# Kernel tuning notes

Hardware: AMD Instinct MI355X
Metric: run time of the kernel (lower is better)

Reference implementation:

```python
import jax, jax.numpy as jnp
import numpy as np

N_NODES = 50000
N_EDGES = 800000
N_GRAPHS = 2048
NODE_F = 30
EDGE_F = 8
HID = 32
HEADS = 4
NEG_SLOPE = 0.2


def _gat_conv(x, src, dst, eattr, W, a_src, a_dst, We, a_edge, b):
    # x: [N, Fin]; src/dst: [E'] (self-loops already appended); eattr: [E', edge_dim]
    N = x.shape[0]
    H, C = a_src.shape
    h = (x @ W).reshape(N, H, C)                     # [N,H,C]
    e = (eattr @ We).reshape(-1, H, C)               # [E',H,C]
    al_s = jnp.sum(h * a_src, axis=-1)               # [N,H]
    al_d = jnp.sum(h * a_dst, axis=-1)               # [N,H]
    al_e = jnp.sum(e * a_edge, axis=-1)              # [E',H]
    alpha = al_s[src] + al_d[dst] + al_e             # [E',H]
    alpha = jax.nn.leaky_relu(alpha, NEG_SLOPE)
    # segment softmax over destination nodes (every node has a self-loop)
    mx = jax.ops.segment_max(alpha, dst, num_segments=N)
    alpha = jnp.exp(alpha - mx[dst])
    den = jax.ops.segment_sum(alpha, dst, num_segments=N)
    alpha = alpha / (den[dst] + 1e-16)
    msg = h[src] * alpha[:, :, None]                 # [E',H,C]
    out = jax.ops.segment_sum(msg, dst, num_segments=N)  # [N,H,C]
    return out.reshape(N, H * C) + b


def _make_params(key):
    ks = jax.random.split(key, 32)
    i = 0
    p = {}
    def nxt(shape, scale=0.1):
        nonlocal i
        k = ks[i]; i += 1
        return jax.random.normal(k, shape, dtype=jnp.float32) * scale
    dims = [(NODE_F, HEADS * HID), (HEADS * HID, HEADS * HID), (HEADS * HID, HEADS * HID)]
    for li, (fin, fout) in enumerate(dims, 1):
        p[f"W{li}"] = nxt((fin, fout))
        p[f"att_src{li}"] = nxt((HEADS, HID))
        p[f"att_dst{li}"] = nxt((HEADS, HID))
        p[f"We{li}"] = nxt((EDGE_F, HEADS * HID))
        p[f"att_e{li}"] = nxt((HEADS, HID))
        p[f"b{li}"] = nxt((HEADS * HID,))
    p["lw1"] = nxt((HEADS * HID, HID)); p["lb1"] = nxt((HID,))
    p["lw2"] = nxt((HID, HID)); p["lb2"] = nxt((HID,))
    p["lw3"] = nxt((HID, 1)); p["lb3"] = nxt((1,))
    return p


def setup_inputs() -> dict:
    key = jax.random.key(0)
    k1, k2, k3, k4, k5 = jax.random.split(key, 5)
    x = jax.random.normal(k1, (N_NODES, NODE_F), dtype=jnp.float32)
    edge_index = jax.random.randint(k2, (2, N_EDGES), 0, N_NODES, dtype=jnp.int64)
    edge_features = jax.random.normal(k3, (N_EDGES, EDGE_F), dtype=jnp.float32)
    batch = jnp.sort(jax.random.randint(k4, (N_NODES,), 0, N_GRAPHS, dtype=jnp.int64))
    inp = {"x": x, "edge_index": edge_index, "edge_features": edge_features, "batch": batch}
    inp.update(_make_params(k5))
    return inp


def reference(x, edge_index, edge_features, batch,
              W1, att_src1, att_dst1, We1, att_e1, b1,
              W2, att_src2, att_dst2, We2, att_e2, b2,
              W3, att_src3, att_dst3, We3, att_e3, b3,
              lw1, lb1, lw2, lb2, lw3, lb3):
    N = x.shape[0]
    # add self-loops (PyG GATConv default); self-loop edge_attr = mean of edge_attr
    loop = jnp.arange(N, dtype=edge_index.dtype)
    src = jnp.concatenate([edge_index[0], loop])
    dst = jnp.concatenate([edge_index[1], loop])
    mean_e = jnp.mean(edge_features, axis=0, keepdims=True)
    eattr = jnp.concatenate([edge_features, jnp.broadcast_to(mean_e, (N, EDGE_F))], axis=0)

    h = jax.nn.relu(_gat_conv(x, src, dst, eattr, W1, att_src1, att_dst1, We1, att_e1, b1))
    h = jax.nn.relu(_gat_conv(h, src, dst, eattr, W2, att_src2, att_dst2, We2, att_e2, b2))
    h = jax.nn.relu(_gat_conv(h, src, dst, eattr, W3, att_src3, att_dst3, We3, att_e3, b3))
    # global_add_pool
    g = jax.ops.segment_sum(h, batch, num_segments=N_GRAPHS)   # [G, H*C]
    g = jax.nn.relu(g @ lw1 + lb1)
    g = jax.nn.relu(g @ lw2 + lb2)
    g = jax.nn.relu(g @ lw3 + lb3)                              # [G, 1]
    return g
```

## Files before the change

kernel.cpp:

```cpp
#include <hip/hip_runtime.h>

#define NND 50000
#define NE  800000
#define NET 850000
#define NG  2048
#define SCB 196
#define MB  1024

typedef __attribute__((ext_vector_type(8))) short short8;
typedef __attribute__((ext_vector_type(4))) float float4v;

__device__ __forceinline__ float frelu(float v){ return v > 0.f ? v : 0.f; }

__device__ __forceinline__ unsigned short f2bf(float f){
    unsigned int u = __float_as_uint(f);
    u += 0x7FFFu + ((u >> 16) & 1u);
    return (unsigned short)(u >> 16);
}

__global__ __launch_bounds__(256) void k_mean(const float4* __restrict__ ef4,
                                              float* __restrict__ partial){
    __shared__ float4 red[256];
    int t = threadIdx.x;
    int i0 = blockIdx.x * 256 + t;
    const int S = MB * 256;
    float4 a = make_float4(0.f, 0.f, 0.f, 0.f);
    for (int j = i0; j < NE * 2; j += S){
        float4 v = ef4[j];
        a.x += v.x; a.y += v.y; a.z += v.z; a.w += v.w;
    }
    red[t] = a;
    __syncthreads();
    for (int off = 128; off >= 2; off >>= 1){
        if (t < off){
            float4 o = red[t + off];
            float4 m = red[t];
            m.x += o.x; m.y += o.y; m.z += o.z; m.w += o.w;
            red[t] = m;
        }
        __syncthreads();
    }
    if (t < 8){
        float v = (t < 4) ? ((const float*)&red[0])[t]
                          : ((const float*)&red[1])[t - 4];
        partial[blockIdx.x * 8 + t] = v;
    }
}

__global__ void k_prep(const float* __restrict__ partial,
                       const float* __restrict__ We1, const float* __restrict__ ae1,
                       const float* __restrict__ We2, const float* __restrict__ ae2,
                       const float* __restrict__ We3, const float* __restrict__ ae3,
                       float* __restrict__ M, float* __restrict__ sc){
    __shared__ float me[8];
    __shared__ float pm[16][8];
    __shared__ float Ms[96];
    int t = threadIdx.x;
    {
        int ch = t & 7, seg = t >> 3;
        float s = 0.f;
        for (int j = seg; j < MB; j += 16) s += partial[j * 8 + ch];
        pm[seg][ch] = s;
    }
    __syncthreads();
    if (t < 8){
        float s = 0.f;
        for (int i = 0; i < 16; i++) s += pm[i][t];
        me[t] = s * (1.0f / NE);
    }
    if (t < 96){
        int l = t >> 5, f = (t >> 2) & 7, h = t & 3;
        const float* We = (l == 0) ? We1 : ((l == 1) ? We2 : We3);
        const float* ae = (l == 0) ? ae1 : ((l == 1) ? ae2 : ae3);
        float s = 0.f;
        for (int c = 0; c < 32; c++) s += We[f * 128 + h * 32 + c] * ae[h * 32 + c];
        M[t] = s; Ms[t] = s;
    }
    __syncthreads();
    if (t < 12){
        int l = t >> 2, h = t & 3;
        float s = 0.f;
        for (int f = 0; f < 8; f++) s += me[f] * Ms[l * 32 + f * 4 + h];
        sc[t] = s;
    }
}

template<int FIN, int FINR>
__global__ __launch_bounds__(256) void k_gemm(
        const float* __restrict__ x, const float* __restrict__ W,
        const float* __restrict__ asrc, const float* __restrict__ adst,
        unsigned short* __restrict__ h, float* __restrict__ als,
        float* __restrict__ ald){
    constexpr int KS = FIN + 8;
    constexpr int SZ1 = 64 * KS + 128 * KS;
    constexpr int SZ2 = 64 * 136;
    constexpr int LSZ = SZ1 > SZ2 ? SZ1 : SZ2;
    __shared__ unsigned short lds[LSZ];
    unsigned short* xa = lds;
    unsigned short* wb = lds + 64 * KS;
    int t = threadIdx.x;
    int r0 = blockIdx.x * 64;

    for (int i = t; i < 64 * (FIN / 2); i += 256){
        int r = i / (FIN / 2), kp = i % (FIN / 2);
        int gr = r0 + r, k = 2 * kp;
        float v0 = 0.f, v1 = 0.f;
        if (gr < NND){
            if (k     < FINR) v0 = x[gr * FINR + k];
            if (k + 1 < FINR) v1 = x[gr * FINR + k + 1];
        }
        unsigned int pk = (unsigned int)f2bf(v0) | ((unsigned int)f2bf(v1) << 16);
        *(unsigned int*)&xa[r * KS + k] = pk;
    }
    for (int i = t; i < 128 * (FIN / 2); i += 256){
        int n = i & 127, kp = i >> 7, k = 2 * kp;
        float v0 = (k     < FINR) ? W[k * 128 + n]       : 0.f;
        float v1 = (k + 1 < FINR) ? W[(k + 1) * 128 + n] : 0.f;
        unsigned int pk = (unsigned int)f2bf(v0) | ((unsigned int)f2bf(v1) << 16);
        *(unsigned int*)&wb[n * KS + k] = pk;
    }
    __syncthreads();

    int wv = t >> 6, lane = t & 63;
    int quad = lane >> 4, lrow = lane & 15;
    int arow = wv * 16 + lrow;
    int koff = quad * 8;
    float4v acc[8];
    #pragma unroll
    for (int nt = 0; nt < 8; nt++) acc[nt] = (float4v){0.f, 0.f, 0.f, 0.f};
    #pragma unroll
    for (int ks = 0; ks < FIN / 32; ks++){
        short8 af = *(const short8*)&xa[arow * KS + ks * 32 + koff];
        #pragma unroll
        for (int nt = 0; nt < 8; nt++){
            short8 bf = *(const short8*)&wb[(nt * 16 + lrow) * KS + ks * 32 + koff];
            acc[nt] = __builtin_amdgcn_mfma_f32_16x16x32_bf16(af, bf, acc[nt], 0, 0, 0);
        }
    }
    __syncthreads();
    unsigned short* hb = lds;
    #pragma unroll
    for (int nt = 0; nt < 8; nt++){
        #pragma unroll
        for (int reg = 0; reg < 4; reg++){
            int lr = wv * 16 + quad * 4 + reg;
            hb[lr * 136 + nt * 16 + lrow] = f2bf(acc[nt][reg]);
        }
    }
    __syncthreads();
    {
        int r = t >> 2, hd = t & 3;
        int gr = r0 + r;
        float sa = 0.f, sd = 0.f;
        const unsigned short* hp = &hb[r * 136 + hd * 32];
        #pragma unroll
        for (int c = 0; c < 32; c++){
            float hv = __uint_as_float(((unsigned int)hp[c]) << 16);
            sa += hv * asrc[hd * 32 + c];
            sd += hv * adst[hd * 32 + c];
        }
        if (gr < NND){ als[gr * 4 + hd] = sa; ald[gr * 4 + hd] = sd; }
    }
    for (int i = t; i < 64 * 16; i += 256){
        int r = i >> 4, c8 = i & 15;
        int gr = r0 + r;
        if (gr < NND)
            *(int4*)&h[gr * 128 + c8 * 8] = *(const int4*)&hb[r * 136 + c8 * 8];
    }
}

__global__ void k_hist(const int* __restrict__ ei, int* __restrict__ cnt,
                       int* __restrict__ pose){
    int e = blockIdx.x * 256 + threadIdx.x;
    if (e >= NE) return;
    int d = ei[NE + e];
    pose[e] = atomicAdd(&cnt[d], 1);
}

__global__ __launch_bounds__(256) void k_scan1(const int* __restrict__ cnt,
                                               int* __restrict__ bsum){
    __shared__ int red[256];
    int t = threadIdx.x;
    int idx = blockIdx.x * 256 + t;
    red[t] = (idx < NND) ? (cnt[idx] + 1) : 0;
    __syncthreads();
    for (int off = 128; off > 0; off >>= 1){
        if (t < off) red[t] += red[t + off];
        __syncthreads();
    }
    if (t == 0) bsum[blockIdx.x] = red[0];
}

__global__ __launch_bounds__(256) void k_scan2(const int* __restrict__ bsum,
                                               int* __restrict__ boff,
                                               int* __restrict__ rs){
    __shared__ int ls[256];
    int t = threadIdx.x;
    int v = (t < SCB) ? bsum[t] : 0;
    ls[t] = v;
    __syncthreads();
    for (int off = 1; off < 256; off <<= 1){
        int u = (t >= off) ? ls[t - off] : 0;
        __syncthreads();
        ls[t] += u;
        __syncthreads();
    }
    if (t < SCB) boff[t] = ls[t] - bsum[t];
    if (t == 0)  rs[NND] = ls[255];
}

__global__ __launch_bounds__(256) void k_scan3(const int* __restrict__ cnt,
                                               const int* __restrict__ boff,
                                               int* __restrict__ rs){
    __shared__ int ls[256];
    int t = threadIdx.x;
    int idx = blockIdx.x * 256 + t;
    int v = (idx < NND) ? (cnt[idx] + 1) : 0;
    ls[t] = v;
    __syncthreads();
    for (int off = 1; off < 256; off <<= 1){
        int u = (t >= off) ? ls[t - off] : 0;
        __syncthreads();
        ls[t] += u;
        __syncthreads();
    }
    if (idx < NND) rs[idx] = boff[blockIdx.x] + ls[t] - v;
}

__global__ void k_scatter(const int* __restrict__ ei, const int* __restrict__ rs,
                          const int* __restrict__ pose, int* __restrict__ srcarr,
                          int* __restrict__ slotof){
    int e = blockIdx.x * 256 + threadIdx.x;
    if (e >= NET) return;
    if (e < NE){
        int s = ei[e], d = ei[NE + e];
        int slot = rs[d] + 1 + pose[e];
        srcarr[slot] = s;
        slotof[e] = slot;
    } else {
        int n = e - NE;
        srcarr[rs[n]] = n;
    }
}

__global__ __launch_bounds__(256) void k_weight(
        const int* __restrict__ ei, const float* __restrict__ ef,
        const float4* __restrict__ als4, const float4* __restrict__ ald4,
        const float* __restrict__ Mg, const float* __restrict__ sc4g,
        const int* __restrict__ rs, const int* __restrict__ slotof,
        float4* __restrict__ wS){
    __shared__ float Ms[32];
    __shared__ float Scs[4];
    int t = threadIdx.x;
    if (t < 32) Ms[t] = Mg[t];
    if (t < 4)  Scs[t] = sc4g[t];
    __syncthreads();
    int e = blockIdx.x * 256 + t;
    if (e < NE){
        int s = ei[e], d = ei[NE + e];
        const float4* efp = (const float4*)ef;
        float4 u = efp[e * 2], v = efp[e * 2 + 1];
        float4 A = als4[s], D = ald4[d];
        float4 w;
        float* wp = &w.x;
        const float* Ap = &A.x; const float* Dp = &D.x;
        #pragma unroll
        for (int h = 0; h < 4; h++){
            float ae = u.x * Ms[0 + h]  + u.y * Ms[4 + h]
                     + u.z * Ms[8 + h]  + u.w * Ms[12 + h]
                     + v.x * Ms[16 + h] + v.y * Ms[20 + h]
                     + v.z * Ms[24 + h] + v.w * Ms[28 + h];
            float a = Ap[h] + Dp[h] + ae;
            a = a > 0.f ? a : 0.2f * a;
            wp[h] = __expf(a);
        }
        wS[slotof[e]] = w;
    } else if (e < NE + NND){
        int n = e - NE;
        float4 A = als4[n], D = ald4[n];
        float4 w;
        float* wp = &w.x;
        const float* Ap = &A.x; const float* Dp = &D.x;
        #pragma unroll
        for (int h = 0; h < 4; h++){
            float a = Ap[h] + Dp[h] + Scs[h];
            a = a > 0.f ? a : 0.2f * a;
            wp[h] = __expf(a);
        }
        wS[rs[n]] = w;
    }
}

__global__ __launch_bounds__(256) void k_gather(
        const int* __restrict__ srcarr, const int* __restrict__ rs,
        const float* __restrict__ wS,
        const unsigned int* __restrict__ HU,
        const float* __restrict__ b, float* __restrict__ out){
    int wid  = threadIdx.x >> 6;
    int lane = threadIdx.x & 63;
    int n = blockIdx.x * 4 + wid;
    int start = rs[n], end = rs[n + 1];
    int cnt = end - start;
    int mh = lane >> 4;
    float ax = 0.f, ay = 0.f, accw = 0.f;

    int s[8]; float w[8];
    int k = 0;
    if (cnt >= 8){
        #pragma unroll
        for (int j = 0; j < 8; j++){
            int i = start + j;
            s[j] = srcarr[i];
            w[j] = wS[i * 4 + mh];
        }
    }
    while (k + 8 <= cnt){
        int cs[8]; float cw[8];
        #pragma unroll
        for (int j = 0; j < 8; j++){ cs[j] = s[j]; cw[j] = w[j]; }
        k += 8;
        if (k + 8 <= cnt){
            #pragma unroll
            for (int j = 0; j < 8; j++){
                int i = start + k + j;
                s[j] = srcarr[i];
                w[j] = wS[i * 4 + mh];
            }
        }
        unsigned int hv[8];
        #pragma unroll
        for (int j = 0; j < 8; j++) hv[j] = HU[cs[j] * 64 + lane];
        #pragma unroll
        for (int j = 0; j < 8; j++){
            float lo = __uint_as_float(hv[j] << 16);
            float hi = __uint_as_float(hv[j] & 0xFFFF0000u);
            ax += cw[j] * lo;
            ay += cw[j] * hi;
            accw += cw[j];
        }
    }
    int rem = cnt - k;
    if (rem > 0){
        int ts[8]; float tw[8];
        #pragma unroll
        for (int j = 0; j < 8; j++){
            bool v = j < rem;
            int i = v ? (start + k + j) : start;
            ts[j] = srcarr[i];
            tw[j] = v ? wS[i * 4 + mh] : 0.f;
        }
        unsigned int hv[8];
        #pragma unroll
        for (int j = 0; j < 8; j++) hv[j] = HU[ts[j] * 64 + lane];
        #pragma unroll
        for (int j = 0; j < 8; j++){
            float lo = __uint_as_float(hv[j] << 16);
            float hi = __uint_as_float(hv[j] & 0xFFFF0000u);
            ax += tw[j] * lo;
            ay += tw[j] * hi;
            accw += tw[j];
        }
    }
    float inv = 1.f / (accw + 1e-16f);
    int c0 = 2 * lane;
    float2 o;
    o.x = frelu(ax * inv + b[c0]);
    o.y = frelu(ay * inv + b[c0 + 1]);
    ((float2*)out)[n * 64 + lane] = o;
}

__global__ __launch_bounds__(128) void k_pool(const float* __restrict__ y,
                                              const int* __restrict__ batch,
                                              float* __restrict__ g){
    int c = threadIdx.x;
    int n0 = blockIdx.x * 32;
    if (n0 >= NND) return;
    int cur = batch[n0];
    float s = 0.f;
    for (int k = 0; k < 32; k++){
        int n = n0 + k;
        if (n >= NND) break;
        int bg = batch[n];
        if (bg != cur){
            atomicAdd(&g[cur * 128 + c], s);
            s = 0.f; cur = bg;
        }
        s += y[n * 128 + c];
    }
    atomicAdd(&g[cur * 128 + c], s);
}

__global__ void k_mlp(const float* __restrict__ g,
                      const float* __restrict__ lw1, const float* __restrict__ lb1,
                      const float* __restrict__ lw2, const float* __restrict__ lb2,
                      const float* __restrict__ lw3, const float* __restrict__ lb3,
                      float* __restrict__ out){
    __shared__ float t1[4][32];
    __shared__ float t2[4][32];
    int tid = threadIdx.x, sub = tid >> 5, j = tid & 31;
    int gi = blockIdx.x * 4 + sub;
    const float* gr = g + gi * 128;
    float s = lb1[j];
    for (int c = 0; c < 128; c++) s += gr[c] * lw1[c * 32 + j];
    t1[sub][j] = frelu(s);
    __syncthreads();
    float s2 = lb2[j];
    for (int k = 0; k < 32; k++) s2 += t1[sub][k] * lw2[k * 32 + j];
    t2[sub][j] = frelu(s2);
    __syncthreads();
    if (j == 0){
        float o = lb3[0];
        for (int k = 0; k < 32; k++) o += t2[sub][k] * lw3[k];
        out[gi] = frelu(o);
    }
}

extern "C" void kernel_launch(void* const* d_in, const int* in_sizes, int n_in,
                              void* d_out, int out_size, void* d_ws, size_t ws_size,
                              hipStream_t stream) {
    const float* x     = (const float*)d_in[0];
    const int*   ei    = (const int*)  d_in[1];
    const float* ef    = (const float*)d_in[2];
    const int*   batch = (const int*)  d_in[3];
    const float* W[3]   = {(const float*)d_in[4],  (const float*)d_in[10], (const float*)d_in[16]};
    const float* as_[3] = {(const float*)d_in[5],  (const float*)d_in[11], (const float*)d_in[17]};
    const float* ad_[3] = {(const float*)d_in[6],  (const float*)d_in[12], (const float*)d_in[18]};
    const float* We[3]  = {(const float*)d_in[7],  (const float*)d_in[13], (const float*)d_in[19]};
    const float* ae[3]  = {(const float*)d_in[8],  (const float*)d_in[14], (const float*)d_in[20]};
    const float* b_[3]  = {(const float*)d_in[9],  (const float*)d_in[15], (const float*)d_in[21]};
    const float* lw1 = (const float*)d_in[22]; const float* lb1 = (const float*)d_in[23];
    const float* lw2 = (const float*)d_in[24]; const float* lb2 = (const float*)d_in[25];
    const float* lw3 = (const float*)d_in[26]; const float* lb3 = (const float*)d_in[27];

    float* ws = (float*)d_ws;
    float* Bx   = ws;
    float* Hbf  = Bx + 6400000;
    float* wSf  = Hbf + 6400000;
    float* als  = wSf + 3400000;
    float* ald  = als + 200000;
    float* g    = ald + 200000;
    float* partial = g + 262144;
    float* M    = partial + MB * 8;
    float* sc   = M + 96;
    int*   srcarr = (int*)(sc + 16);
    int*   slotof = srcarr + NET;
    int*   pose   = slotof + NE;
    int*   rs     = pose + NE;
    int*   cnt    = rs + NND + 4;
    int*   bsum   = cnt + NND;
    int*   boff   = bsum + SCB;

    unsigned short* Hb = (unsigned short*)Hbf;

    hipMemsetAsync(cnt, 0, NND * sizeof(int), stream);
    hipMemsetAsync(g,   0, NG * 128 * sizeof(float), stream);

    k_mean<<<MB, 256, 0, stream>>>((const float4*)ef, partial);
    k_prep<<<1, 128, 0, stream>>>(partial, We[0], ae[0], We[1], ae[1], We[2], ae[2], M, sc);

    k_hist<<<(NE + 255) / 256, 256, 0, stream>>>(ei, cnt, pose);
    k_scan1<<<SCB, 256, 0, stream>>>(cnt, bsum);
    k_scan2<<<1, 256, 0, stream>>>(bsum, boff, rs);
    k_scan3<<<SCB, 256, 0, stream>>>(cnt, boff, rs);
    k_scatter<<<(NET + 255) / 256, 256, 0, stream>>>(ei, rs, pose, srcarr, slotof);

    const int GB = (NND + 63) / 64;
    const float* xin = x;
    for (int l = 0; l < 3; l++){
        if (l == 0)
            k_gemm<32, 30><<<GB, 256, 0, stream>>>(xin, W[l], as_[l], ad_[l],
                                                   Hb, als, ald);
        else
            k_gemm<128, 128><<<GB, 256, 0, stream>>>(xin, W[l], as_[l], ad_[l],
                                                     Hb, als, ald);
        k_weight<<<(NE + NND + 255) / 256, 256, 0, stream>>>(
            ei, ef, (const float4*)als, (const float4*)ald,
            M + l * 32, sc + l * 4, rs, slotof, (float4*)wSf);
        k_gather<<<NND / 4, 256, 0, stream>>>(srcarr, rs, wSf,
                                              (const unsigned int*)Hb, b_[l], Bx);
        xin = Bx;
    }

    k_pool<<<(NND + 31) / 32, 128, 0, stream>>>(Bx, batch, g);
    k_mlp<<<NG / 4, 128, 0, stream>>>(g, lw1, lb1, lw2, lb2, lw3, lb3, (float*)d_out);
}
```

Before: 472.6 us.

## Fuse attention weight computation into gather, store activations as bf16, fold memsets

Removes the separate per-edge weight kernel and its intermediate weight buffer: the gather kernel now reads (src, edge id) pairs and recomputes each edge's attention weight inline from the edge features, als and ald. Layer outputs are written as packed bf16 so the next GEMM loads them directly and pooling reads half the bytes. The two memsets are folded into the mean kernel. The cost is redundant per-lane work: each of the 4 head groups of 16 lanes recomputes the same edge weight. Edge-feature reads are also now random instead of coalesced, and the stored activations lose precision.

```diff
diff --git a/kernel.cpp b/kernel.cpp
--- a/kernel.cpp
+++ b/kernel.cpp
@@ -17,12 +17,28 @@
     u += 0x7FFFu + ((u >> 16) & 1u);
     return (unsigned short)(u >> 16);
 }
+__device__ __forceinline__ float bf2f(unsigned short s){
+    return __uint_as_float(((unsigned int)s) << 16);
+}
+__device__ __forceinline__ float sel4(float4 v, int m){
+    float r = v.x;
+    r = (m == 1) ? v.y : r;
+    r = (m == 2) ? v.z : r;
+    r = (m == 3) ? v.w : r;
+    return r;
+}
+
+struct MC { float m[8]; };
 
 __global__ __launch_bounds__(256) void k_mean(const float4* __restrict__ ef4,
-                                              float* __restrict__ partial){
+                                              float* __restrict__ partial,
+                                              float* __restrict__ gz,
+                                              int* __restrict__ cntz){
     __shared__ float4 red[256];
     int t = threadIdx.x;
     int i0 = blockIdx.x * 256 + t;
+    gz[i0] = 0.f;
+    if (i0 < NND) cntz[i0] = 0;
     const int S = MB * 256;
     float4 a = make_float4(0.f, 0.f, 0.f, 0.f);
     for (int j = i0; j < NE * 2; j += S){
@@ -85,9 +101,9 @@
     }
 }
 
-template<int FIN, int FINR>
+template<int FIN, int FINR, int BFIN>
 __global__ __launch_bounds__(256) void k_gemm(
-        const float* __restrict__ x, const float* __restrict__ W,
+        const void* __restrict__ xv, const float* __restrict__ W,
         const float* __restrict__ asrc, const float* __restrict__ adst,
         unsigned short* __restrict__ h, float* __restrict__ als,
         float* __restrict__ ald){
@@ -101,16 +117,27 @@
     int t = threadIdx.x;
     int r0 = blockIdx.x * 64;
 
-    for (int i = t; i < 64 * (FIN / 2); i += 256){
-        int r = i / (FIN / 2), kp = i % (FIN / 2);
-        int gr = r0 + r, k = 2 * kp;
-        float v0 = 0.f, v1 = 0.f;
-        if (gr < NND){
-            if (k     < FINR) v0 = x[gr * FINR + k];
-            if (k + 1 < FINR) v1 = x[gr * FINR + k + 1];
-        }
-        unsigned int pk = (unsigned int)f2bf(v0) | ((unsigned int)f2bf(v1) << 16);
-        *(unsigned int*)&xa[r * KS + k] = pk;
+    if (BFIN){
+        const unsigned int* xu = (const unsigned int*)xv;
+        for (int i = t; i < 64 * (FIN / 2); i += 256){
+            int r = i / (FIN / 2), kp = i % (FIN / 2);
+            int gr = r0 + r;
+            unsigned int pk = (gr < NND) ? xu[gr * (FINR / 2) + kp] : 0u;
+            *(unsigned int*)&xa[r * KS + 2 * kp] = pk;
+        }
+    } else {
+        const float* x = (const float*)xv;
+        for (int i = t; i < 64 * (FIN / 2); i += 256){
+            int r = i / (FIN / 2), kp = i % (FIN / 2);
+            int gr = r0 + r, k = 2 * kp;
+            float v0 = 0.f, v1 = 0.f;
+            if (gr < NND){
+                if (k     < FINR) v0 = x[gr * FINR + k];
+                if (k + 1 < FINR) v1 = x[gr * FINR + k + 1];
+            }
+            unsigned int pk = (unsigned int)f2bf(v0) | ((unsigned int)f2bf(v1) << 16);
+            *(unsigned int*)&xa[r * KS + k] = pk;
+        }
     }
     for (int i = t; i < 128 * (FIN / 2); i += 256){
         int n = i & 127, kp = i >> 7, k = 2 * kp;
@@ -155,7 +182,7 @@
         const unsigned short* hp = &hb[r * 136 + hd * 32];
         #pragma unroll
         for (int c = 0; c < 32; c++){
-            float hv = __uint_as_float(((unsigned int)hp[c]) << 16);
+            float hv = bf2f(hp[c]);
             sa += hv * asrc[hd * 32 + c];
             sd += hv * adst[hd * 32 + c];
         }
@@ -228,104 +255,80 @@
 }
 
 __global__ void k_scatter(const int* __restrict__ ei, const int* __restrict__ rs,
-                          const int* __restrict__ pose, int* __restrict__ srcarr,
-                          int* __restrict__ slotof){
+                          const int* __restrict__ pose, int2* __restrict__ se){
     int e = blockIdx.x * 256 + threadIdx.x;
     if (e >= NET) return;
     if (e < NE){
         int s = ei[e], d = ei[NE + e];
-        int slot = rs[d] + 1 + pose[e];
-        srcarr[slot] = s;
-        slotof[e] = slot;
+        se[rs[d] + 1 + pose[e]] = make_int2(s, e);
     } else {
         int n = e - NE;
-        srcarr[rs[n]] = n;
-    }
-}
-
-__global__ __launch_bounds__(256) void k_weight(
-        const int* __restrict__ ei, const float* __restrict__ ef,
+        se[rs[n]] = make_int2(n, -1);
+    }
+}
+
+__device__ __forceinline__ float edge_w(int src, int eid,
+        const float4* __restrict__ ef4, const float4* __restrict__ als4,
+        const MC& mc, float scv, float aldv, int mh){
+    float aeh;
+    if (eid >= 0){
+        float4 u = ef4[eid * 2], v = ef4[eid * 2 + 1];
+        aeh = u.x * mc.m[0] + u.y * mc.m[1] + u.z * mc.m[2] + u.w * mc.m[3]
+            + v.x * mc.m[4] + v.y * mc.m[5] + v.z * mc.m[6] + v.w * mc.m[7];
+    } else {
+        aeh = scv;
+    }
+    float a = sel4(als4[src], mh) + aldv + aeh;
+    a = a > 0.f ? a : 0.2f * a;
+    return __expf(a);
+}
+
+__global__ __launch_bounds__(256) void k_gather(
+        const int2* __restrict__ se, const int* __restrict__ rs,
+        const float4* __restrict__ ef4,
         const float4* __restrict__ als4, const float4* __restrict__ ald4,
         const float* __restrict__ Mg, const float* __restrict__ sc4g,
-        const int* __restrict__ rs, const int* __restrict__ slotof,
-        float4* __restrict__ wS){
+        const unsigned int* __restrict__ HU,
+        const float* __restrict__ b, unsigned int* __restrict__ outU){
     __shared__ float Ms[32];
     __shared__ float Scs[4];
     int t = threadIdx.x;
     if (t < 32) Ms[t] = Mg[t];
     if (t < 4)  Scs[t] = sc4g[t];
     __syncthreads();
-    int e = blockIdx.x * 256 + t;
-    if (e < NE){
-        int s = ei[e], d = ei[NE + e];
-        const float4* efp = (const float4*)ef;
-        float4 u = efp[e * 2], v = efp[e * 2 + 1];
-        float4 A = als4[s], D = ald4[d];
-        float4 w;
-        float* wp = &w.x;
-        const float* Ap = &A.x; const float* Dp = &D.x;
-        #pragma unroll
-        for (int h = 0; h < 4; h++){
-            float ae = u.x * Ms[0 + h]  + u.y * Ms[4 + h]
-                     + u.z * Ms[8 + h]  + u.w * Ms[12 + h]
-                     + v.x * Ms[16 + h] + v.y * Ms[20 + h]
-                     + v.z * Ms[24 + h] + v.w * Ms[28 + h];
-            float a = Ap[h] + Dp[h] + ae;
-            a = a > 0.f ? a : 0.2f * a;
-            wp[h] = __expf(a);
-        }
-        wS[slotof[e]] = w;
-    } else if (e < NE + NND){
-        int n = e - NE;
-        float4 A = als4[n], D = ald4[n];
-        float4 w;
-        float* wp = &w.x;
-        const float* Ap = &A.x; const float* Dp = &D.x;
-        #pragma unroll
-        for (int h = 0; h < 4; h++){
-            float a = Ap[h] + Dp[h] + Scs[h];
-            a = a > 0.f ? a : 0.2f * a;
-            wp[h] = __expf(a);
-        }
-        wS[rs[n]] = w;
-    }
-}
-
-__global__ __launch_bounds__(256) void k_gather(
-        const int* __restrict__ srcarr, const int* __restrict__ rs,
-        const float* __restrict__ wS,
-        const unsigned int* __restrict__ HU,
-        const float* __restrict__ b, float* __restrict__ out){
-    int wid  = threadIdx.x >> 6;
-    int lane = threadIdx.x & 63;
+    int wid  = t >> 6;
+    int lane = t & 63;
     int n = blockIdx.x * 4 + wid;
     int start = rs[n], end = rs[n + 1];
     int cnt = end - start;
     int mh = lane >> 4;
+    MC mc;
+    #pragma unroll
+    for (int f = 0; f < 8; f++) mc.m[f] = Ms[f * 4 + mh];
+    float scv  = Scs[mh];
+    float aldv = sel4(ald4[n], mh);
     float ax = 0.f, ay = 0.f, accw = 0.f;
 
-    int s[8]; float w[8];
+    int2 sj[8]; float w[8];
     int k = 0;
     if (cnt >= 8){
         #pragma unroll
-        for (int j = 0; j < 8; j++){
-            int i = start + j;
-            s[j] = srcarr[i];
-            w[j] = wS[i * 4 + mh];
-        }
+        for (int j = 0; j < 8; j++) sj[j] = se[start + j];
+        #pragma unroll
+        for (int j = 0; j < 8; j++)
+            w[j] = edge_w(sj[j].x, sj[j].y, ef4, als4, mc, scv, aldv, mh);
     }
     while (k + 8 <= cnt){
         int cs[8]; float cw[8];
         #pragma unroll
-        for (int j = 0; j < 8; j++){ cs[j] = s[j]; cw[j] = w[j]; }
+        for (int j = 0; j < 8; j++){ cs[j] = sj[j].x; cw[j] = w[j]; }
         k += 8;
         if (k + 8 <= cnt){
             #pragma unroll
-            for (int j = 0; j < 8; j++){
-                int i = start + k + j;
-                s[j] = srcarr[i];
-                w[j] = wS[i * 4 + mh];
-            }
+            for (int j = 0; j < 8; j++) sj[j] = se[start + k + j];
+            #pragma unroll
+            for (int j = 0; j < 8; j++)
+                w[j] = edge_w(sj[j].x, sj[j].y, ef4, als4, mc, scv, aldv, mh);
         }
         unsigned int hv[8];
         #pragma unroll
@@ -346,8 +349,10 @@
         for (int j = 0; j < 8; j++){
             bool v = j < rem;
             int i = v ? (start + k + j) : start;
-            ts[j] = srcarr[i];
-            tw[j] = v ? wS[i * 4 + mh] : 0.f;
+            int2 p = se[i];
+            ts[j] = p.x;
+            float wj = edge_w(p.x, p.y, ef4, als4, mc, scv, aldv, mh);
+            tw[j] = v ? wj : 0.f;
         }
         unsigned int hv[8];
         #pragma unroll
@@ -363,13 +368,12 @@
     }
     float inv = 1.f / (accw + 1e-16f);
     int c0 = 2 * lane;
-    float2 o;
-    o.x = frelu(ax * inv + b[c0]);
-    o.y = frelu(ay * inv + b[c0 + 1]);
-    ((float2*)out)[n * 64 + lane] = o;
-}
-
-__global__ __launch_bounds__(128) void k_pool(const float* __restrict__ y,
+    float ox = frelu(ax * inv + b[c0]);
+    float oy = frelu(ay * inv + b[c0 + 1]);
+    outU[n * 64 + lane] = (unsigned int)f2bf(ox) | ((unsigned int)f2bf(oy) << 16);
+}
+
+__global__ __launch_bounds__(128) void k_pool(const unsigned short* __restrict__ y,
                                               const int* __restrict__ batch,
                                               float* __restrict__ g){
     int c = threadIdx.x;
@@ -385,7 +389,7 @@
             atomicAdd(&g[cur * 128 + c], s);
             s = 0.f; cur = bg;
         }
-        s += y[n * 128 + c];
+        s += bf2f(y[n * 128 + c]);
     }
     atomicAdd(&g[cur * 128 + c], s);
 }
@@ -435,52 +439,45 @@
     float* ws = (float*)d_ws;
     float* Bx   = ws;
     float* Hbf  = Bx + 6400000;
-    float* wSf  = Hbf + 6400000;
-    float* als  = wSf + 3400000;
+    float* als  = Hbf + 6400000;
     float* ald  = als + 200000;
     float* g    = ald + 200000;
     float* partial = g + 262144;
     float* M    = partial + MB * 8;
     float* sc   = M + 96;
-    int*   srcarr = (int*)(sc + 16);
-    int*   slotof = srcarr + NET;
-    int*   pose   = slotof + NE;
-    int*   rs     = pose + NE;
-    int*   cnt    = rs + NND + 4;
-    int*   bsum   = cnt + NND;
-    int*   boff   = bsum + SCB;
+    int2*  se   = (int2*)(sc + 16);
+    int*   pose = (int*)(se + NET);
+    int*   rs   = pose + NE;
+    int*   cnt  = rs + NND + 4;
+    int*   bsum = cnt + NND;
+    int*   boff = bsum + SCB;
 
     unsigned short* Hb = (unsigned short*)Hbf;
 
-    hipMemsetAsync(cnt, 0, NND * sizeof(int), stream);
-    hipMemsetAsync(g,   0, NG * 128 * sizeof(float), stream);
-
-    k_mean<<<MB, 256, 0, stream>>>((const float4*)ef, partial);
+    k_mean<<<MB, 256, 0, stream>>>((const float4*)ef, partial, g, cnt);
     k_prep<<<1, 128, 0, stream>>>(partial, We[0], ae[0], We[1], ae[1], We[2], ae[2], M, sc);
 
     k_hist<<<(NE + 255) / 256, 256, 0, stream>>>(ei, cnt, pose);
     k_scan1<<<SCB, 256, 0, stream>>>(cnt, bsum);
     k_scan2<<<1, 256, 0, stream>>>(bsum, boff, rs);
     k_scan3<<<SCB, 256, 0, stream>>>(cnt, boff, rs);
-    k_scatter<<<(NET + 255) / 256, 256, 0, stream>>>(ei, rs, pose, srcarr, slotof);
+    k_scatter<<<(NET + 255) / 256, 256, 0, stream>>>(ei, rs, pose, se);
 
     const int GB = (NND + 63) / 64;
-    const float* xin = x;
     for (int l = 0; l < 3; l++){
         if (l == 0)
-            k_gemm<32, 30><<<GB, 256, 0, stream>>>(xin, W[l], as_[l], ad_[l],
-                                                   Hb, als, ald);
+            k_gemm<32, 30, 0><<<GB, 256, 0, stream>>>(x, W[l], as_[l], ad_[l],
+                                                      Hb, als, ald);
         else
-            k_gemm<128, 128><<<GB, 256, 0, stream>>>(xin, W[l], as_[l], ad_[l],
-                                                     Hb, als, ald);
-        k_weight<<<(NE + NND + 255) / 256, 256, 0, stream>>>(
-            ei, ef, (const float4*)als, (const float4*)ald,
-            M + l * 32, sc + l * 4, rs, slotof, (float4*)wSf);
-        k_gather<<<NND / 4, 256, 0, stream>>>(srcarr, rs, wSf,
-                                              (const unsigned int*)Hb, b_[l], Bx);
-        xin = Bx;
-    }
-
-    k_pool<<<(NND + 31) / 32, 128, 0, stream>>>(Bx, batch, g);
+            k_gemm<128, 128, 1><<<GB, 256, 0, stream>>>(Bx, W[l], as_[l], ad_[l],
+                                                        Hb, als, ald);
+        k_gather<<<NND / 4, 256, 0, stream>>>(se, rs, (const float4*)ef,
+                                              (const float4*)als, (const float4*)ald,
+                                              M + l * 32, sc + l * 4,
+                                              (const unsigned int*)Hb, b_[l],
+                                              (unsigned int*)Bx);
+    }
+
+    k_pool<<<(NND + 31) / 32, 128, 0, stream>>>((const unsigned short*)Bx, batch, g);
     k_mlp<<<NG / 4, 128, 0, stream>>>(g, lw1, lb1, lw2, lb2, lw3, lb3, (float*)d_out);
 }
```

Result: slower. 823.1 us (+74.2%).
